# Kernel tuning notes

Measured on AMD Instinct MI355X. Metric: run time of the kernel, lower is better.

The kernel has to match this reference:

```python
import jax, jax.numpy as jnp
import numpy as np

N_NODES = 16384   # total nodes
B = 32            # graphs in batch
NPG = 512         # nodes per graph (uniform -> dense mask is all True)
E = 262144        # edges (avg degree 16)
H = 64            # hidden_dim
HEADS = 8
DH = H // HEADS


def setup_inputs() -> dict:
    key = jax.random.key(0)
    ks = jax.random.split(key, 20)
    x = jax.random.normal(ks[0], (N_NODES, H), dtype=jnp.float32)
    # edges constrained within each graph of 512 nodes
    src = jax.random.randint(ks[1], (E,), 0, N_NODES, dtype=jnp.int32)
    dst = (src // NPG) * NPG + jax.random.randint(ks[2], (E,), 0, NPG, dtype=jnp.int32)
    edge_index = jnp.stack([src, dst])
    batch = (jnp.arange(N_NODES, dtype=jnp.int32) // NPG)
    c_size = jnp.full((B,), NPG, dtype=jnp.int32)
    s = 1.0 / np.sqrt(H)
    p = lambda k, shape: (jax.random.normal(k, shape, dtype=jnp.float32) * s)
    return {
        "x": x,
        "w_gat": p(ks[3], (H, H)), "att_src": p(ks[4], (H,)), "att_dst": p(ks[5], (H,)), "b_gat": jnp.zeros((H,), jnp.float32),
        "g1": jnp.ones((H,), jnp.float32), "b1": jnp.zeros((H,), jnp.float32),
        "wq": p(ks[6], (H, H)), "bq": jnp.zeros((H,), jnp.float32),
        "wk": p(ks[7], (H, H)), "bk": jnp.zeros((H,), jnp.float32),
        "wv": p(ks[8], (H, H)), "bv": jnp.zeros((H,), jnp.float32),
        "wo": p(ks[9], (H, H)), "bo": jnp.zeros((H,), jnp.float32),
        "g2": jnp.ones((H,), jnp.float32), "b2": jnp.zeros((H,), jnp.float32),
        "edge_index": edge_index, "batch": batch, "c_size": c_size,
    }


def _layer_norm(x, g, b):
    mu = jnp.mean(x, axis=-1, keepdims=True)
    var = jnp.var(x, axis=-1, keepdims=True)
    return (x - mu) * jax.lax.rsqrt(var + 1e-5) * g + b


def _gat_conv(x, edge_index, w, a_src, a_dst, bias):
    # PyG GATConv, 1 head, add_self_loops=True, leaky_relu slope 0.2
    n = x.shape[0]
    loops = jnp.arange(n, dtype=edge_index.dtype)
    src = jnp.concatenate([edge_index[0], loops])
    dst = jnp.concatenate([edge_index[1], loops])
    h = x @ w                                  # [n, H]
    e = jax.nn.leaky_relu((h @ a_src)[src] + (h @ a_dst)[dst], 0.2)  # [E+n]
    m = jax.ops.segment_max(e, dst, num_segments=n)
    p = jnp.exp(e - m[dst])
    s = jax.ops.segment_sum(p, dst, num_segments=n)
    alpha = p / (s[dst] + 1e-16)
    out = jax.ops.segment_sum(alpha[:, None] * h[src], dst, num_segments=n)
    return out + bias


def reference(x, w_gat, att_src, att_dst, b_gat, g1, b1,
              wq, bq, wk, bk, wv, bv, wo, bo, g2, b2,
              edge_index, batch, c_size):
    # GAT branch (dropout is identity in eval)
    x_ = jax.nn.relu(_gat_conv(x, edge_index, w_gat, att_src, att_dst, b_gat))
    x1 = _layer_norm(x + x_, g1, b1)                     # [n, H]
    # to_dense_batch: uniform graphs -> mask all True, plain reshape
    xd = x1.reshape(B, NPG, H)
    q = (xd @ wq + bq).reshape(B, NPG, HEADS, DH)
    k = (xd @ wk + bk).reshape(B, NPG, HEADS, DH)
    v = (xd @ wv + bv).reshape(B, NPG, HEADS, DH)
    scores = jnp.einsum('bqhd,bkhd->bhqk', q, k) / np.sqrt(DH)  # [B,h,N,N]
    attn = jax.nn.softmax(scores, axis=-1)
    o = jnp.einsum('bhqk,bkhd->bqhd', attn, v).reshape(B, NPG, H)
    o = o @ wo + bo
    x2 = _layer_norm(x1 + jax.nn.relu(o.reshape(N_NODES, H)), g2, b2)
    return x2  # recon_loss is None in eval mode
```

## Files before the change

### kernel.cpp

```cpp
#include <hip/hip_runtime.h>
#include <hip/hip_bf16.h>

#define NN     16384
#define HD     64
#define BG     32
#define NPG    512
#define NHEADS 8
#define DH     8
#define DEGMAX 40

#define KVSTR  20
#define CSTR   (64 * KVSTR + 4)
#define QSTR   12

typedef __hip_bfloat16 bf16;

__device__ __forceinline__ float b2f(bf16 v) { return __bfloat162float(v); }

__device__ __forceinline__ float ldf(const void* p, int i, int bf) {
  return bf ? __bfloat162float(((const bf16*)p)[i]) : ((const float*)p)[i];
}

__device__ __forceinline__ float wave_sum(float v) {
#pragma unroll
  for (int off = 32; off > 0; off >>= 1) v += __shfl_xor(v, off);
  return v;
}

__device__ __forceinline__ void unpack8(uint4 u, float* f) {
  f[0] = __uint_as_float(u.x << 16); f[1] = __uint_as_float(u.x & 0xffff0000u);
  f[2] = __uint_as_float(u.y << 16); f[3] = __uint_as_float(u.y & 0xffff0000u);
  f[4] = __uint_as_float(u.z << 16); f[5] = __uint_as_float(u.z & 0xffff0000u);
  f[6] = __uint_as_float(u.w << 16); f[7] = __uint_as_float(u.w & 0xffff0000u);
}

__device__ __forceinline__ unsigned short bfbits(float f) {
  bf16 b = __float2bfloat16(f);
  return *(unsigned short*)&b;
}

__device__ __forceinline__ int detect_bf(const unsigned short* xr, int tid, int nt) {
  __shared__ int s_cnt;
  if (tid == 0) s_cnt = 0;
  __syncthreads();
  int sane = 0;
  for (int i = tid; i < 2048; i += nt) {
    int e = (xr[2 * i] >> 7) & 0xFF;
    sane += (e >= 100 && e <= 150) ? 1 : 0;
  }
  if (sane) atomicAdd(&s_cnt, sane);
  __syncthreads();
  return s_cnt > 1400;
}

__global__ __launch_bounds__(256) void k_build(
    const void* __restrict__ x, const void* __restrict__ w,
    const void* __restrict__ asrc, const void* __restrict__ adst,
    const int* __restrict__ esrc, const int* __restrict__ edst, int E,
    int* __restrict__ cur, int* __restrict__ ell,
    bf16* __restrict__ h, float* __restrict__ as_, float* __restrict__ ad_,
    int* __restrict__ flagp)
{
  const int tid = threadIdx.x, lane = tid & 63, wid = tid >> 6;
  const int bf = detect_bf((const unsigned short*)x, tid, 256);
  if (tid == 0 && blockIdx.x == 0) *flagp = bf;
  __shared__ float wl[HD * HD];
  __shared__ float xr[4][HD];
  {
    for (int e = blockIdx.x * 256 + tid; e < E; e += gridDim.x * 256) {
      int d = edst[e];
      int k = atomicAdd(&cur[d], 1);
      if (k < DEGMAX) ell[d * DEGMAX + k] = esrc[e];
    }
  }
  for (int i = tid; i < HD * HD; i += 256) wl[i] = ldf(w, i, bf);
  const float av = ldf(asrc, lane, bf), dv_ = ldf(adst, lane, bf);
  __syncthreads();
#pragma unroll
  for (int r = 0; r < 4; ++r) {
    const int node = blockIdx.x * 16 + r * 4 + wid;
    xr[wid][lane] = ldf(x, node * HD + lane, bf);
    float hj = 0.f;
#pragma unroll
    for (int i = 0; i < HD; ++i) hj = fmaf(xr[wid][i], wl[i * HD + lane], hj);
    float pa = wave_sum(hj * av);
    float pd = wave_sum(hj * dv_);
    h[node * HD + lane] = __float2bfloat16(hj);
    if (lane == 0) { as_[node] = pa; ad_[node] = pd; }
  }
}

__global__ __launch_bounds__(256) void k_gather(
    const void* __restrict__ x, const int* __restrict__ cur,
    const int* __restrict__ ell, const float* __restrict__ as_,
    const float* __restrict__ ad_, const bf16* __restrict__ h,
    const void* __restrict__ bg, const void* __restrict__ g1,
    const void* __restrict__ b1, const int* __restrict__ dflag,
    bf16* __restrict__ x1)
{
  const int tid = threadIdx.x, lane = tid & 63, wid = tid >> 6;
  const int bf = *dflag;
  const int n = blockIdx.x * 4 + wid;
  const float adn = ad_[n];
  float e0 = as_[n] + adn;
  e0 = e0 > 0.f ? e0 : 0.2f * e0;
  float den = __expf(fminf(e0, 30.f));
  float num = den * b2f(h[n * HD + lane]);
  const int deg = min(cur[n], DEGMAX);
  const int* row = ell + n * DEGMAX;
  int i = 0;
  for (; i + 4 <= deg; i += 4) {
    int s0 = row[i], s1 = row[i + 1], s2 = row[i + 2], s3 = row[i + 3];
    float a0 = as_[s0], a1 = as_[s1], a2 = as_[s2], a3 = as_[s3];
    float h0 = b2f(h[s0 * HD + lane]), h1 = b2f(h[s1 * HD + lane]);
    float h2 = b2f(h[s2 * HD + lane]), h3 = b2f(h[s3 * HD + lane]);
    float e_0 = a0 + adn; e_0 = e_0 > 0.f ? e_0 : 0.2f * e_0;
    float e_1 = a1 + adn; e_1 = e_1 > 0.f ? e_1 : 0.2f * e_1;
    float e_2 = a2 + adn; e_2 = e_2 > 0.f ? e_2 : 0.2f * e_2;
    float e_3 = a3 + adn; e_3 = e_3 > 0.f ? e_3 : 0.2f * e_3;
    float p0 = __expf(fminf(e_0, 30.f)), p1 = __expf(fminf(e_1, 30.f));
    float p2 = __expf(fminf(e_2, 30.f)), p3 = __expf(fminf(e_3, 30.f));
    den += p0 + p1 + p2 + p3;
    num = fmaf(p0, h0, num); num = fmaf(p1, h1, num);
    num = fmaf(p2, h2, num); num = fmaf(p3, h3, num);
  }
  for (; i < deg; ++i) {
    int s = row[i];
    float e = as_[s] + adn;
    e = e > 0.f ? e : 0.2f * e;
    float p = __expf(fminf(e, 30.f));
    den += p;
    num = fmaf(p, b2f(h[s * HD + lane]), num);
  }
  float v = num / (den + 1e-16f) + ldf(bg, lane, bf);
  v = fmaxf(v, 0.f) + ldf(x, n * HD + lane, bf);
  float mu = wave_sum(v) * (1.f / 64.f);
  float dv = v - mu;
  float var = wave_sum(dv * dv) * (1.f / 64.f);
  float r = rsqrtf(var + 1e-5f);
  x1[n * HD + lane] =
      __float2bfloat16(dv * r * ldf(g1, lane, bf) + ldf(b1, lane, bf));
}

__global__ __launch_bounds__(512, 2) void k_attn10(
    const bf16* __restrict__ x1,
    const void* __restrict__ wq, const void* __restrict__ bq,
    const void* __restrict__ wk, const void* __restrict__ bk,
    const void* __restrict__ wv, const void* __restrict__ bv,
    const int* __restrict__ dflag,
    bf16* __restrict__ num_t, float* __restrict__ den_t)
{
  const int t = threadIdx.x;
  const int bf = *dflag;
  __shared__ float KV[4 * CSTR];
  __shared__ float Q[NPG * QSTR];
  __shared__ float Wl[3][HD][DH];
  __shared__ float bl[3][DH];
  const int bid = blockIdx.x;
  const int g = bid >> 4, hd = (bid >> 1) & 7, half = bid & 1;
  {
    int i = t >> 3, j = t & 7;
    int col = hd * DH + j;
    Wl[0][i][j] = ldf(wq, i * HD + col, bf);
    Wl[1][i][j] = ldf(wk, i * HD + col, bf);
    Wl[2][i][j] = ldf(wv, i * HD + col, bf);
    if (t < DH) {
      bl[0][t] = ldf(bq, hd * DH + t, bf);
      bl[1][t] = ldf(bk, hd * DH + t, bf);
      bl[2][t] = ldf(bv, hd * DH + t, bf);
    }
  }
  __syncthreads();
  const float qscale = 0.3535533905932738f * 1.4426950408889634f;
  if (t < 256) {
    const uint4* xk4 = (const uint4*)(x1 + (size_t)(g * NPG + half * 256 + t) * HD);
    float kr[DH], vr[DH];
#pragma unroll
    for (int j = 0; j < DH; ++j) { kr[j] = bl[1][j]; vr[j] = bl[2][j]; }
#pragma unroll
    for (int blk = 0; blk < 8; ++blk) {
      float xv[8];
      unpack8(xk4[blk], xv);
      const int ib = blk * 8;
#pragma unroll
      for (int ii = 0; ii < 8; ++ii)
#pragma unroll
        for (int j = 0; j < DH; ++j) {
          kr[j] = fmaf(xv[ii], Wl[1][ib + ii][j], kr[j]);
          vr[j] = fmaf(xv[ii], Wl[2][ib + ii][j], vr[j]);
        }
    }
    float* kvrow = KV + (t >> 6) * CSTR + (t & 63) * KVSTR;
    *(float4*)(kvrow +  0) = make_float4(kr[0], kr[1], kr[2], kr[3]);
    *(float4*)(kvrow +  4) = make_float4(kr[4], kr[5], kr[6], kr[7]);
    *(float4*)(kvrow +  8) = make_float4(vr[0], vr[1], vr[2], vr[3]);
    *(float4*)(kvrow + 12) = make_float4(vr[4], vr[5], vr[6], vr[7]);
  } else {
    const int tq = t - 256;
    const uint4* xa4 = (const uint4*)(x1 + (size_t)(g * NPG + tq) * HD);
    const uint4* xb4 = (const uint4*)(x1 + (size_t)(g * NPG + tq + 256) * HD);
    float qa[DH], qb[DH];
#pragma unroll
    for (int j = 0; j < DH; ++j) { qa[j] = bl[0][j]; qb[j] = bl[0][j]; }
#pragma unroll
    for (int blk = 0; blk < 8; ++blk) {
      float xva[8], xvb[8];
      unpack8(xa4[blk], xva);
      unpack8(xb4[blk], xvb);
      const int ib = blk * 8;
#pragma unroll
      for (int ii = 0; ii < 8; ++ii)
#pragma unroll
        for (int j = 0; j < DH; ++j) {
          qa[j] = fmaf(xva[ii], Wl[0][ib + ii][j], qa[j]);
          qb[j] = fmaf(xvb[ii], Wl[0][ib + ii][j], qb[j]);
        }
    }
    float* q0 = Q + tq * QSTR;
    float* q1 = Q + (tq + 256) * QSTR;
    *(float4*)(q0 + 0) = make_float4(qa[0] * qscale, qa[1] * qscale, qa[2] * qscale, qa[3] * qscale);
    *(float4*)(q0 + 4) = make_float4(qa[4] * qscale, qa[5] * qscale, qa[6] * qscale, qa[7] * qscale);
    *(float4*)(q1 + 0) = make_float4(qb[0] * qscale, qb[1] * qscale, qb[2] * qscale, qb[3] * qscale);
    *(float4*)(q1 + 4) = make_float4(qb[4] * qscale, qb[5] * qscale, qb[6] * qscale, qb[7] * qscale);
  }
  __syncthreads();
  const int qg = t >> 3, c = t & 7;
  float qv[8][DH];
#pragma unroll
  for (int i = 0; i < 8; ++i) {
    const float* qrow = Q + (qg * 8 + i) * QSTR;
    float4 a = *(const float4*)(qrow);
    float4 b = *(const float4*)(qrow + 4);
    qv[i][0] = a.x; qv[i][1] = a.y; qv[i][2] = a.z; qv[i][3] = a.w;
    qv[i][4] = b.x; qv[i][5] = b.y; qv[i][6] = b.z; qv[i][7] = b.w;
  }
  float den[8], num[8][DH];
#pragma unroll
  for (int i = 0; i < 8; ++i) {
    den[i] = 0.f;
#pragma unroll
    for (int j = 0; j < DH; ++j) num[i][j] = 0.f;
  }
  const float* kvc = KV + (c >> 1) * CSTR + (c & 1) * 32 * KVSTR;
  for (int jj = 0; jj < 32; ++jj) {
    const float4* kv4 = (const float4*)(kvc + jj * KVSTR);
    float4 k0 = kv4[0], k1 = kv4[1], v0 = kv4[2], v1 = kv4[3];
#pragma unroll
    for (int i = 0; i < 8; ++i) {
      float s = qv[i][0] * k0.x;
      s = fmaf(qv[i][1], k0.y, s); s = fmaf(qv[i][2], k0.z, s);
      s = fmaf(qv[i][3], k0.w, s); s = fmaf(qv[i][4], k1.x, s);
      s = fmaf(qv[i][5], k1.y, s); s = fmaf(qv[i][6], k1.z, s);
      s = fmaf(qv[i][7], k1.w, s);
      float p = exp2f(s);
      den[i] += p;
      num[i][0] = fmaf(p, v0.x, num[i][0]); num[i][1] = fmaf(p, v0.y, num[i][1]);
      num[i][2] = fmaf(p, v0.z, num[i][2]); num[i][3] = fmaf(p, v0.w, num[i][3]);
      num[i][4] = fmaf(p, v1.x, num[i][4]); num[i][5] = fmaf(p, v1.y, num[i][5]);
      num[i][6] = fmaf(p, v1.z, num[i][6]); num[i][7] = fmaf(p, v1.w, num[i][7]);
    }
  }
#pragma unroll
  for (int st = 1; st <= 4; st <<= 1) {
#pragma unroll
    for (int i = 0; i < 8; ++i) {
      den[i] += __shfl_xor(den[i], st);
#pragma unroll
      for (int j = 0; j < DH; ++j) num[i][j] += __shfl_xor(num[i][j], st);
    }
  }
  float dsel = 0.f, rsel[DH];
#pragma unroll
  for (int j = 0; j < DH; ++j) rsel[j] = 0.f;
#pragma unroll
  for (int i = 0; i < 8; ++i) {
    if (c == i) {
      dsel = den[i];
#pragma unroll
      for (int j = 0; j < DH; ++j) rsel[j] = num[i][j];
    }
  }
  const int qrow = qg * 8 + c;
  const int plane = half * 8 + hd;
  union { uint4 u4; unsigned short us[8]; } pk;
#pragma unroll
  for (int j = 0; j < DH; ++j) pk.us[j] = bfbits(rsel[j]);
  *(uint4*)(num_t + ((size_t)plane * NN + g * NPG + qrow) * 8) = pk.u4;
  den_t[(size_t)plane * NN + g * NPG + qrow] = dsel;
}

__global__ __launch_bounds__(256) void k_out(
    const bf16* __restrict__ num_t, const float* __restrict__ den_t,
    const bf16* __restrict__ x1,
    const void* __restrict__ wo, const void* __restrict__ bo,
    const void* __restrict__ g2, const void* __restrict__ b2,
    const int* __restrict__ dflag, void* __restrict__ out)
{
  const int tid = threadIdx.x, lane = tid & 63, wid = tid >> 6;
  const int bf = *dflag;
  __shared__ float wl[HD * HD];
  __shared__ float orow[4][HD];
  for (int i = tid; i < HD * HD; i += 256) wl[i] = ldf(wo, i, bf);
  const float bov = ldf(bo, lane, bf);
  const float g2v = ldf(g2, lane, bf);
  const float b2v = ldf(b2, lane, bf);
  const int hdp = lane >> 3, jp = lane & 7;
  __syncthreads();
#pragma unroll
  for (int r = 0; r < 4; ++r) {
    const int node = blockIdx.x * 16 + r * 4 + wid;
    {
      float nm = b2f(num_t[((size_t)hdp * NN + node) * 8 + jp]) +
                 b2f(num_t[((size_t)(8 + hdp) * NN + node) * 8 + jp]);
      float dn = den_t[(size_t)hdp * NN + node] +
                 den_t[(size_t)(8 + hdp) * NN + node];
      orow[wid][lane] = nm / dn;
    }
    float y = bov;
#pragma unroll
    for (int i = 0; i < HD; ++i) y = fmaf(orow[wid][i], wl[i * HD + lane], y);
    float tt = b2f(x1[node * HD + lane]) + fmaxf(y, 0.f);
    float mu = wave_sum(tt) * (1.f / 64.f);
    float dv = tt - mu;
    float var = wave_sum(dv * dv) * (1.f / 64.f);
    float rr = rsqrtf(var + 1e-5f);
    float res = dv * rr * g2v + b2v;
    if (bf) ((bf16*)out)[node * HD + lane] = __float2bfloat16(res);
    else    ((float*)out)[node * HD + lane] = res;
  }
}

extern "C" void kernel_launch(void* const* d_in, const int* in_sizes, int n_in,
                              void* d_out, int out_size, void* d_ws, size_t ws_size,
                              hipStream_t stream)
{
  const void* x    = d_in[0];
  const void* wgat = d_in[1];
  const void* asrc = d_in[2];
  const void* adst = d_in[3];
  const void* bgat = d_in[4];
  const void* g1   = d_in[5];
  const void* b1   = d_in[6];
  const void* wq   = d_in[7];
  const void* bq   = d_in[8];
  const void* wk   = d_in[9];
  const void* bk   = d_in[10];
  const void* wv   = d_in[11];
  const void* bv   = d_in[12];
  const void* wo   = d_in[13];
  const void* bo   = d_in[14];
  const void* g2   = d_in[15];
  const void* b2   = d_in[16];
  const int*  ei   = (const int*)d_in[17];
  const int E = in_sizes[17] / 2;
  const int* esrc = ei;
  const int* edst = ei + E;

  char* W = (char*)d_ws;
  bf16*  x1b   = (bf16*)W;
  int*   ell   = (int*)(W + (size_t)(2 << 20));
  bf16*  hb    = (bf16*)(W + (size_t)(2 << 20) + (size_t)NN * DEGMAX * 4);
  bf16*  num_t = (bf16*)(W + (size_t)(2 << 20));
  float* den_t = (float*)(W + (size_t)(6 << 20));
  float* as_   = (float*)(W + (size_t)(7 << 20));
  float* ad_   = as_ + NN;
  int*   cur   = (int*)(ad_ + NN);
  int*   flag  = cur + NN;

  hipMemsetAsync(cur, 0, NN * sizeof(int), stream);
  k_build  <<<NN / 16, 256, 0, stream>>>(x, wgat, asrc, adst, esrc, edst, E,
                                         cur, ell, hb, as_, ad_, flag);
  k_gather <<<NN / 4, 256, 0, stream>>>(x, cur, ell, as_, ad_, hb,
                                        bgat, g1, b1, flag, x1b);
  k_attn10 <<<BG * NHEADS * 2, 512, 0, stream>>>(x1b, wq, bq, wk, bk, wv, bv,
                                                 flag, num_t, den_t);
  k_out    <<<NN / 16, 256, 0, stream>>>(num_t, den_t, x1b, wo, bo, g2, b2,
                                         flag, d_out);
}
```

Measured before the change: 213.4 us.

## Regroup KV smem chunks, use hardware exp2, unroll gather by 8, shrink dtype probe

Splits the 256 keys staged in shared memory into 8 chunks of 32 instead of 4 of 64, so each of the 8 column lanes reads its own contiguous chunk, which changes the bank-conflict pattern. The softmax exponent now uses the raw amdgcn exp2 builtin, skipping the library range handling. The GAT neighbour gather gets an 8-wide unrolled loop to issue more independent loads at once. The bf16 detection probe samples fewer elements with a scaled threshold, which cuts startup work but makes the dtype guess slightly less robust.

```diff
diff --git a/kernel.cpp b/kernel.cpp
--- a/kernel.cpp
+++ b/kernel.cpp
@@ -10,10 +10,20 @@
 #define DEGMAX 40
 
 #define KVSTR  20
-#define CSTR   (64 * KVSTR + 4)
+#define CSTR   (32 * KVSTR + 4)
 #define QSTR   12
 
 typedef __hip_bfloat16 bf16;
+
+#if defined(__has_builtin)
+#if __has_builtin(__builtin_amdgcn_exp2f)
+#define EXP2F(x) __builtin_amdgcn_exp2f(x)
+#else
+#define EXP2F(x) exp2f(x)
+#endif
+#else
+#define EXP2F(x) exp2f(x)
+#endif
 
 __device__ __forceinline__ float b2f(bf16 v) { return __bfloat162float(v); }
 
@@ -44,13 +54,13 @@
   if (tid == 0) s_cnt = 0;
   __syncthreads();
   int sane = 0;
-  for (int i = tid; i < 2048; i += nt) {
+  for (int i = tid; i < 512; i += nt) {
     int e = (xr[2 * i] >> 7) & 0xFF;
     sane += (e >= 100 && e <= 150) ? 1 : 0;
   }
   if (sane) atomicAdd(&s_cnt, sane);
   __syncthreads();
-  return s_cnt > 1400;
+  return s_cnt > 350;
 }
 
 __global__ __launch_bounds__(256) void k_build(
@@ -109,6 +119,24 @@
   const int deg = min(cur[n], DEGMAX);
   const int* row = ell + n * DEGMAX;
   int i = 0;
+  for (; i + 8 <= deg; i += 8) {
+    int s[8];
+#pragma unroll
+    for (int k = 0; k < 8; ++k) s[k] = row[i + k];
+    float a[8], hh[8];
+#pragma unroll
+    for (int k = 0; k < 8; ++k) a[k] = as_[s[k]];
+#pragma unroll
+    for (int k = 0; k < 8; ++k) hh[k] = b2f(h[s[k] * HD + lane]);
+#pragma unroll
+    for (int k = 0; k < 8; ++k) {
+      float e = a[k] + adn;
+      e = e > 0.f ? e : 0.2f * e;
+      float p = __expf(fminf(e, 30.f));
+      den += p;
+      num = fmaf(p, hh[k], num);
+    }
+  }
   for (; i + 4 <= deg; i += 4) {
     int s0 = row[i], s1 = row[i + 1], s2 = row[i + 2], s3 = row[i + 3];
     float a0 = as_[s0], a1 = as_[s1], a2 = as_[s2], a3 = as_[s3];
@@ -142,7 +170,7 @@
       __float2bfloat16(dv * r * ldf(g1, lane, bf) + ldf(b1, lane, bf));
 }
 
-__global__ __launch_bounds__(512, 2) void k_attn10(
+__global__ __launch_bounds__(512, 2) void k_attn12(
     const bf16* __restrict__ x1,
     const void* __restrict__ wq, const void* __restrict__ bq,
     const void* __restrict__ wk, const void* __restrict__ bk,
@@ -152,7 +180,7 @@
 {
   const int t = threadIdx.x;
   const int bf = *dflag;
-  __shared__ float KV[4 * CSTR];
+  __shared__ float KV[8 * CSTR];
   __shared__ float Q[NPG * QSTR];
   __shared__ float Wl[3][HD][DH];
   __shared__ float bl[3][DH];
@@ -190,7 +218,7 @@
           vr[j] = fmaf(xv[ii], Wl[2][ib + ii][j], vr[j]);
         }
     }
-    float* kvrow = KV + (t >> 6) * CSTR + (t & 63) * KVSTR;
+    float* kvrow = KV + (t >> 5) * CSTR + (t & 31) * KVSTR;
     *(float4*)(kvrow +  0) = make_float4(kr[0], kr[1], kr[2], kr[3]);
     *(float4*)(kvrow +  4) = make_float4(kr[4], kr[5], kr[6], kr[7]);
     *(float4*)(kvrow +  8) = make_float4(vr[0], vr[1], vr[2], vr[3]);
@@ -241,7 +269,7 @@
 #pragma unroll
     for (int j = 0; j < DH; ++j) num[i][j] = 0.f;
   }
-  const float* kvc = KV + (c >> 1) * CSTR + (c & 1) * 32 * KVSTR;
+  const float* kvc = KV + c * CSTR;
   for (int jj = 0; jj < 32; ++jj) {
     const float4* kv4 = (const float4*)(kvc + jj * KVSTR);
     float4 k0 = kv4[0], k1 = kv4[1], v0 = kv4[2], v1 = kv4[3];
@@ -252,7 +280,7 @@
       s = fmaf(qv[i][3], k0.w, s); s = fmaf(qv[i][4], k1.x, s);
       s = fmaf(qv[i][5], k1.y, s); s = fmaf(qv[i][6], k1.z, s);
       s = fmaf(qv[i][7], k1.w, s);
-      float p = exp2f(s);
+      float p = EXP2F(s);
       den[i] += p;
       num[i][0] = fmaf(p, v0.x, num[i][0]); num[i][1] = fmaf(p, v0.y, num[i][1]);
       num[i][2] = fmaf(p, v0.z, num[i][2]); num[i][3] = fmaf(p, v0.w, num[i][3]);
@@ -372,7 +400,7 @@
                                          cur, ell, hb, as_, ad_, flag);
   k_gather <<<NN / 4, 256, 0, stream>>>(x, cur, ell, as_, ad_, hb,
                                         bgat, g1, b1, flag, x1b);
-  k_attn10 <<<BG * NHEADS * 2, 512, 0, stream>>>(x1b, wq, bq, wk, bk, wv, bv,
+  k_attn12 <<<BG * NHEADS * 2, 512, 0, stream>>>(x1b, wq, bq, wk, bk, wv, bv,
                                                  flag, num_t, den_t);
   k_out    <<<NN / 16, 256, 0, stream>>>(num_t, den_t, x1b, wo, bo, g2, b2,
                                          flag, d_out);
```

Result: faster. 202.1 us (-5.3%).
